# Optimization experiments

Hardware: AMD Instinct MI355X
Metric: run time of the kernel (lower is better)

The kernel has to match this reference:

```python
import jax, jax.numpy as jnp
import numpy as np

B, N, D_IN, D, K, H, ITERS = 128, 4096, 64, 64, 8, 128, 3
SCALE = D ** -0.5
EPS_ATTN = 1e-8
EPS_LN = 1e-5


def layer_norm(x, g, b):
    m = jnp.mean(x, axis=-1, keepdims=True)
    v = jnp.mean((x - m) ** 2, axis=-1, keepdims=True)
    return (x - m) * jax.lax.rsqrt(v + EPS_LN) * g + b


def setup_inputs() -> dict:
    key = jax.random.key(0)
    ks = jax.random.split(key, 16)
    s = 0.05
    return {
        "inputs": jax.random.normal(ks[0], (B, N, D_IN), dtype=jnp.float32),
        "noise": jax.random.normal(ks[1], (B, K, D), dtype=jnp.float32),
        "slots_mu": jax.random.normal(ks[2], (1, 1, D), dtype=jnp.float32),
        "slots_sigma": jax.random.normal(ks[3], (1, 1, D), dtype=jnp.float32),
        "Wq": jax.random.normal(ks[4], (D, D), dtype=jnp.float32) * s,
        "Wk": jax.random.normal(ks[5], (D_IN, D), dtype=jnp.float32) * s,
        "Wv": jax.random.normal(ks[6], (D_IN, D), dtype=jnp.float32) * s,
        "W_ih": jax.random.normal(ks[7], (3 * D, D), dtype=jnp.float32) * s,
        "W_hh": jax.random.normal(ks[8], (3 * D, D), dtype=jnp.float32) * s,
        "b_ih": jnp.zeros((3 * D,), dtype=jnp.float32),
        "b_hh": jnp.zeros((3 * D,), dtype=jnp.float32),
        "mlp_W1": jax.random.normal(ks[9], (D, H), dtype=jnp.float32) * s,
        "mlp_b1": jnp.zeros((H,), dtype=jnp.float32),
        "mlp_W2": jax.random.normal(ks[10], (H, D), dtype=jnp.float32) * s,
        "mlp_b2": jnp.zeros((D,), dtype=jnp.float32),
        "ln_in_g": jnp.ones((D_IN,), dtype=jnp.float32),
        "ln_in_b": jnp.zeros((D_IN,), dtype=jnp.float32),
        "ln_s_g": jnp.ones((D,), dtype=jnp.float32),
        "ln_s_b": jnp.zeros((D,), dtype=jnp.float32),
        "ln_ff_g": jnp.ones((D,), dtype=jnp.float32),
        "ln_ff_b": jnp.zeros((D,), dtype=jnp.float32),
    }


def reference(inputs, noise, slots_mu, slots_sigma, Wq, Wk, Wv,
              W_ih, W_hh, b_ih, b_hh, mlp_W1, mlp_b1, mlp_W2, mlp_b2,
              ln_in_g, ln_in_b, ln_s_g, ln_s_b, ln_ff_g, ln_ff_b):
    # slots = Normal(mu, sigma) with externally supplied standard noise
    slots = slots_mu + slots_sigma * noise                      # [B,K,D]
    x = layer_norm(inputs, ln_in_g, ln_in_b)                     # [B,N,D_IN]
    k = x @ Wk                                                   # [B,N,D]
    v = x @ Wv                                                   # [B,N,D]

    for _ in range(ITERS):
        slots_prev = slots
        s = layer_norm(slots, ln_s_g, ln_s_b)
        q = s @ Wq                                               # [B,K,D]
        dots = jnp.einsum('bid,bjd->bij', q, k) * SCALE          # [B,K,N]
        attn = jax.nn.softmax(dots, axis=1) + EPS_ATTN           # softmax over slots
        attn_n = attn / jnp.sum(attn, axis=-1, keepdims=True)
        updates = jnp.einsum('bjd,bij->bid', v, attn_n)          # [B,K,D]

        # single-step GRU (torch nn.GRU gate order: reset, update, new)
        gx = updates @ W_ih.T + b_ih                             # [B,K,3D]
        gh = slots_prev @ W_hh.T + b_hh                          # [B,K,3D]
        gx_r, gx_z, gx_n = jnp.split(gx, 3, axis=-1)
        gh_r, gh_z, gh_n = jnp.split(gh, 3, axis=-1)
        r = jax.nn.sigmoid(gx_r + gh_r)
        z = jax.nn.sigmoid(gx_z + gh_z)
        n = jnp.tanh(gx_n + r * gh_n)
        slots = (1.0 - z) * n + z * slots_prev

        slots = layer_norm(slots, ln_ff_g, ln_ff_b)
        slots = slots + (jax.nn.relu(slots @ mlp_W1 + mlp_b1) @ mlp_W2 + mlp_b2)
    return slots
```

## Files before the change

### kernel.cpp

```cpp
#include <hip/hip_runtime.h>
#include <hip/hip_bf16.h>

typedef unsigned int u32;
typedef unsigned short u16;
typedef __attribute__((ext_vector_type(8))) short short8;
typedef __attribute__((ext_vector_type(4))) float f32x4;
typedef __attribute__((ext_vector_type(2))) u32 u32x2;

#define B_      128
#define N_      4096
#define K_      8
#define SCALE_  0.125f
#define EPS_A   1e-8f
#define EPS_LN  1e-5f

__device__ __forceinline__ float bf_lo(u32 u){ union{u32 v; float f;} x; x.v = u<<16; return x.f; }
__device__ __forceinline__ u16 f2bf(float f){
  union{float f; u32 v;} x; x.f = f;
  u32 v = x.v;
  return (u16)((v + 0x7fffu + ((v>>16)&1u))>>16);
}
__device__ __forceinline__ float wsum64(float v){
  #pragma unroll
  for (int off=32; off; off>>=1) v += __shfl_xor(v, off, 64);
  return v;
}
__device__ __forceinline__ void gll16(const void* g, void* l){
  __builtin_amdgcn_global_load_lds(
      (const __attribute__((address_space(1))) void*)g,
      (__attribute__((address_space(3))) void*)l, 16, 0, 0);
}

__global__ void prep_t(const float* __restrict__ Wih, const float* __restrict__ Whh,
                       const float* __restrict__ Wq,  const float* __restrict__ Wk,
                       float* __restrict__ WihT, float* __restrict__ WhhT,
                       float* __restrict__ Wqk){
  int t = threadIdx.x;
  if (blockIdx.x < 48){
    int idx = blockIdx.x*256 + t;
    int g = idx>>6, d = idx&63;
    WihT[d*192+g] = Wih[idx];
    WhhT[d*192+g] = Whh[idx];
  } else {
    __shared__ float WkL[64*65];
    int bi = blockIdx.x - 48;
    #pragma unroll
    for (int k=0;k<16;++k){
      int idx = t + k*256;
      int d = idx>>6, m = idx&63;
      WkL[m*65+d] = Wk[idx];
    }
    __syncthreads();
    int a = bi*4 + (t>>6), d = t&63;
    float acc = 0.f;
    #pragma unroll 8
    for (int m=0;m<64;++m) acc += Wq[a*64+m]*WkL[m*65+d];
    Wqk[a*64+d] = acc;
  }
}

__device__ __forceinline__ void tile_attn(
    char* ibuf, char* abuf, short8 qf0, short8 qf1,
    int fr, int fq, f32x4* c2, float* tsl)
{
  f32x4 c1[2];
  #pragma unroll
  for (int nt=0;nt<2;++nt){
    c1[nt] = (f32x4){0.f,0.f,0.f,0.f};
    #pragma unroll
    for (int kk=0;kk<2;++kk){
      int byte = ((kk*2+(fq>>1))<<10) | (((fr>>2)&1)<<9)
               | ((nt*2+(fr>>3))<<7) | ((fr&3)<<5) | ((fq&1)<<4);
      short8 xf = *(const short8*)(ibuf + byte);
      c1[nt] = __builtin_amdgcn_mfma_f32_16x16x32_bf16(kk?qf1:qf0, xf, c1[nt], 0,0,0);
    }
  }
  #pragma unroll
  for (int nt=0;nt<2;++nt){
    float d0 = c1[nt][0]*SCALE_, d1 = c1[nt][1]*SCALE_;
    float d2 = c1[nt][2]*SCALE_, d3 = c1[nt][3]*SCALE_;
    float m = fmaxf(fmaxf(d0,d1), fmaxf(d2,d3));
    m = fmaxf(m, __shfl_xor(m, 16, 64));
    float e0 = __expf(d0-m), e1 = __expf(d1-m), e2 = __expf(d2-m), e3 = __expf(d3-m);
    float sl = e0+e1+e2+e3;
    float inv = 1.f/(sl + __shfl_xor(sl, 16, 64));
    float a0 = e0*inv + EPS_A, a1 = e1*inv + EPS_A;
    float a2 = e2*inv + EPS_A, a3 = e3*inv + EPS_A;
    tsl[0]+=a0; tsl[1]+=a1; tsl[2]+=a2; tsl[3]+=a3;
    int pos2 = (nt*16 + fr)*2;
    *(u16*)(abuf + (((fq*4+0)*64 + pos2) ^ (0<<4))) = f2bf(a0);
    *(u16*)(abuf + (((fq*4+1)*64 + pos2) ^ (1<<4))) = f2bf(a1);
    *(u16*)(abuf + (((fq*4+2)*64 + pos2) ^ (2<<4))) = f2bf(a2);
    *(u16*)(abuf + (((fq*4+3)*64 + pos2) ^ (3<<4))) = f2bf(a3);
  }
  asm volatile("s_waitcnt lgkmcnt(0)" ::: "memory");
  __builtin_amdgcn_sched_barrier(0);
  {
    short8 pa = *(const short8*)(abuf + ((fr*64 + fq*16) ^ ((fr&3)<<4)));
    u32 va = (u32)(size_t)ibuf + (fq<<7) + (fr<<1);
    u32x2 tv0,tv1,tv2,tv3,tv4,tv5,tv6,tv7;
    asm volatile("ds_read_b64_tr_b16 %0, %1 offset:0"    : "=v"(tv0) : "v"(va));
    asm volatile("ds_read_b64_tr_b16 %0, %1 offset:512"  : "=v"(tv1) : "v"(va));
    asm volatile("ds_read_b64_tr_b16 %0, %1 offset:1024" : "=v"(tv2) : "v"(va));
    asm volatile("ds_read_b64_tr_b16 %0, %1 offset:1536" : "=v"(tv3) : "v"(va));
    asm volatile("ds_read_b64_tr_b16 %0, %1 offset:2048" : "=v"(tv4) : "v"(va));
    asm volatile("ds_read_b64_tr_b16 %0, %1 offset:2560" : "=v"(tv5) : "v"(va));
    asm volatile("ds_read_b64_tr_b16 %0, %1 offset:3072" : "=v"(tv6) : "v"(va));
    asm volatile("ds_read_b64_tr_b16 %0, %1 offset:3584" : "=v"(tv7) : "v"(va));
    asm volatile("s_waitcnt lgkmcnt(0)" ::: "memory");
    __builtin_amdgcn_sched_barrier(0);
    union { short8 s8; u32 u4[4]; } xb;
    xb.u4[0]=tv0.x; xb.u4[1]=tv0.y; xb.u4[2]=tv1.x; xb.u4[3]=tv1.y;
    c2[0] = __builtin_amdgcn_mfma_f32_16x16x32_bf16(pa, xb.s8, c2[0], 0,0,0);
    xb.u4[0]=tv2.x; xb.u4[1]=tv2.y; xb.u4[2]=tv3.x; xb.u4[3]=tv3.y;
    c2[1] = __builtin_amdgcn_mfma_f32_16x16x32_bf16(pa, xb.s8, c2[1], 0,0,0);
    xb.u4[0]=tv4.x; xb.u4[1]=tv4.y; xb.u4[2]=tv5.x; xb.u4[3]=tv5.y;
    c2[2] = __builtin_amdgcn_mfma_f32_16x16x32_bf16(pa, xb.s8, c2[2], 0,0,0);
    xb.u4[0]=tv6.x; xb.u4[1]=tv6.y; xb.u4[2]=tv7.x; xb.u4[3]=tv7.y;
    c2[3] = __builtin_amdgcn_mfma_f32_16x16x32_bf16(pa, xb.s8, c2[3], 0,0,0);
  }
}

__global__ __launch_bounds__(512,1) void fused_sa(
    const float* __restrict__ inp, u16* __restrict__ xhat,
    const float* __restrict__ noise, const float* __restrict__ mu, const float* __restrict__ sigma,
    const float* __restrict__ Wqk,
    const float* __restrict__ lng, const float* __restrict__ lnb,
    const float* __restrict__ lnsg, const float* __restrict__ lnsb,
    const float* __restrict__ WihT, const float* __restrict__ WhhT,
    const float* __restrict__ bih, const float* __restrict__ bhh,
    const float* __restrict__ W1, const float* __restrict__ b1,
    const float* __restrict__ W2, const float* __restrict__ b2,
    const float* __restrict__ lnffg, const float* __restrict__ lnffb,
    const float* __restrict__ Wv,
    float* __restrict__ dout)
{
  __shared__ __align__(16) char smem[152320];
  int b = blockIdx.x, t = threadIdx.x;
  int w = t>>6, lane = t&63;
  int fr = lane&15, fq = lane>>4;
  int i = w, d = lane;

  char*  wbase = smem + w*9216;
  char*  abuf  = wbase + 8192;
  char*  qA    = smem + 73728;
  float* UL    = (float*)(smem + 75776);
  float* SL    = (float*)(smem + 92160);
  u16*   wih_l = (u16*)(smem + 92416);
  u16*   whh_l = (u16*)(smem + 116992);
  float* updL  = (float*)(smem + 141568);
  float* spL   = (float*)(smem + 143744);
  float* sfL   = (float*)(smem + 145920);
  float* hL    = (float*)(smem + 148096);

  {
    const float4* wa = (const float4*)WihT;
    const float4* wb = (const float4*)WhhT;
    #pragma unroll
    for (int k2=0;k2<6;++k2){
      int idx = t + k2*512;
      float4 va = wa[idx], vb = wb[idx];
      ((u32*)wih_l)[idx*2]   = (u32)f2bf(va.x) | ((u32)f2bf(va.y)<<16);
      ((u32*)wih_l)[idx*2+1] = (u32)f2bf(va.z) | ((u32)f2bf(va.w)<<16);
      ((u32*)whh_l)[idx*2]   = (u32)f2bf(vb.x) | ((u32)f2bf(vb.y)<<16);
      ((u32*)whh_l)[idx*2+1] = (u32)f2bf(vb.z) | ((u32)f2bf(vb.w)<<16);
    }
  }
  if (t < 256) ((u32*)(qA + 1024))[t] = 0;
  float sp = mu[d] + sigma[d]*noise[b*512 + t];
  {
    float m  = wsum64(sp)*(1.f/64.f);
    float df = sp - m;
    float vv = wsum64(df*df)*(1.f/64.f);
    float sv = df*rsqrtf(vv+EPS_LN)*lnsg[d] + lnsb[d];
    updL[i*68+d] = sv;
  }
  __syncthreads();
  {
    float qt = 0.f;
    #pragma unroll 8
    for (int dd=0; dd<64; ++dd) qt += updL[i*68+dd]*Wqk[dd*64 + d];
    *(u16*)(qA + ((i*128 + d*2) ^ ((i&7)<<4))) = f2bf(qt);
  }
  __syncthreads();

  long tbase = (long)b*128 + w*16;

  for (int it=0; it<3; ++it){
    f32x4 c2[4];
    #pragma unroll
    for (int k2=0;k2<4;++k2) c2[k2] = (f32x4){0.f,0.f,0.f,0.f};
    float tsl[4] = {0.f,0.f,0.f,0.f};
    short8 qf0 = *(const short8*)(qA + ((fr*128 +  0 + fq*16) ^ ((fr&7)<<4)));
    short8 qf1 = *(const short8*)(qA + ((fr*128 + 64 + fq*16) ^ ((fr&7)<<4)));

    if (it == 0){
      for (int tile=0; tile<16; ++tile){
        char* ibuf = wbase;
        {
          int r = lane>>1, h = lane&1;
          const float4* xr = (const float4*)(inp + ((long)b*N_ + w*512 + tile*32 + r)*64 + h*32);
          float xv[32]; float s=0.f, sq=0.f;
          #pragma unroll
          for (int c=0;c<8;++c){
            float4 f = xr[c];
            xv[c*4+0]=f.x; xv[c*4+1]=f.y; xv[c*4+2]=f.z; xv[c*4+3]=f.w;
            s  += f.x+f.y+f.z+f.w;
            sq += f.x*f.x+f.y*f.y+f.z*f.z+f.w*f.w;
          }
          s  += __shfl_xor(s,1,64);
          sq += __shfl_xor(sq,1,64);
          float mean = s*(1.f/64.f);
          float inv  = rsqrtf(sq*(1.f/64.f) - mean*mean + EPS_LN);
          float lgv[32], lbv[32];
          {
            const float4* g4 = (const float4*)(lng + h*32);
            const float4* b4 = (const float4*)(lnb + h*32);
            #pragma unroll
            for (int e=0;e<8;++e){
              float4 gv = g4[e], bv = b4[e];
              lgv[e*4+0]=gv.x; lgv[e*4+1]=gv.y; lgv[e*4+2]=gv.z; lgv[e*4+3]=gv.w;
              lbv[e*4+0]=bv.x; lbv[e*4+1]=bv.y; lbv[e*4+2]=bv.z; lbv[e*4+3]=bv.w;
            }
          }
          u32 pk[16];
          #pragma unroll
          for (int e=0;e<16;++e){
            float a0 = (xv[e*2]  -mean)*inv*lgv[e*2]   + lbv[e*2];
            float a1 = (xv[e*2+1]-mean)*inv*lgv[e*2+1] + lbv[e*2+1];
            pk[e] = (u32)f2bf(a0) | ((u32)f2bf(a1)<<16);
          }
          int pbits = (((r>>2)&1)<<9) | (((r>>3)&3)<<7) | ((r&3)<<5);
          #pragma unroll
          for (int half=0; half<2; ++half){
            int dt = h*2 + half;
            uint4 v0; v0.x=pk[half*8+0]; v0.y=pk[half*8+1]; v0.z=pk[half*8+2]; v0.w=pk[half*8+3];
            uint4 v1; v1.x=pk[half*8+4]; v1.y=pk[half*8+5]; v1.z=pk[half*8+6]; v1.w=pk[half*8+7];
            *(uint4*)(ibuf + ((dt<<10) | pbits))      = v0;
            *(uint4*)(ibuf + ((dt<<10) | pbits) + 16) = v1;
          }
          asm volatile("s_waitcnt lgkmcnt(0)" ::: "memory");
          __builtin_amdgcn_sched_barrier(0);
          char* gim = (char*)xhat + ((tbase+tile)<<12) + lane*16;
          #pragma unroll
          for (int j=0;j<4;++j)
            *(uint4*)(gim + j*1024) = *(const uint4*)(ibuf + lane*16 + j*1024);
        }
        tile_attn(ibuf, abuf, qf0, qf1, fr, fq, c2, tsl);
      }
      asm volatile("s_waitcnt vmcnt(0)" ::: "memory");
      __builtin_amdgcn_sched_barrier(0);
    } else {
      {
        const char* g0 = (const char*)xhat + (tbase<<12) + lane*16;
        #pragma unroll
        for (int j=0;j<4;++j) gll16(g0 + j*1024, wbase + j*1024);
      }
      #pragma unroll 2
      for (int tile=0; tile<16; ++tile){
        char* ibuf = wbase + (tile&1)*4096;
        if (tile < 15){
          const char* gn = (const char*)xhat + ((tbase+tile+1)<<12) + lane*16;
          char* ln = wbase + ((tile+1)&1)*4096;
          #pragma unroll
          for (int j=0;j<4;++j) gll16(gn + j*1024, ln + j*1024);
          asm volatile("s_waitcnt vmcnt(4)" ::: "memory");
        } else {
          asm volatile("s_waitcnt vmcnt(0)" ::: "memory");
        }
        __builtin_amdgcn_sched_barrier(0);
        tile_attn(ibuf, abuf, qf0, qf1, fr, fq, c2, tsl);
      }
    }
    if (fq < 2){
      #pragma unroll
      for (int dblk=0;dblk<4;++dblk){
        #pragma unroll
        for (int r=0;r<4;++r)
          UL[w*512 + (fq*4+r)*64 + dblk*16 + fr] = c2[dblk][r];
      }
    }
    #pragma unroll
    for (int mk=1; mk<16; mk<<=1){
      tsl[0] += __shfl_xor(tsl[0], mk, 64);
      tsl[1] += __shfl_xor(tsl[1], mk, 64);
      tsl[2] += __shfl_xor(tsl[2], mk, 64);
      tsl[3] += __shfl_xor(tsl[3], mk, 64);
    }
    if (fr==0 && fq<2){
      SL[w*8 + fq*4+0] = tsl[0]; SL[w*8 + fq*4+1] = tsl[1];
      SL[w*8 + fq*4+2] = tsl[2]; SL[w*8 + fq*4+3] = tsl[3];
    }
    __syncthreads();

    float u = 0.f, S = 0.f;
    #pragma unroll
    for (int cw=0; cw<8; ++cw){
      u += UL[cw*512 + i*64 + d];
      S += SL[cw*8 + i];
    }
    float ut = u / S;
    sfL[i*68+d] = ut;
    spL[i*68+d] = sp;
    __syncthreads();
    float upd = 0.f;
    #pragma unroll 8
    for (int dd=0; dd<64; ++dd) upd += sfL[i*68+dd]*Wv[dd*64 + d];
    updL[i*68+d] = upd;
    __syncthreads();
    float gx0 = bih[d], gx1 = bih[64+d], gx2 = bih[128+d];
    float gh0 = bhh[d], gh1 = bhh[64+d], gh2 = bhh[128+d];
    #pragma unroll 8
    for (int dd=0; dd<64; ++dd){
      float uv = updL[i*68+dd];
      float sv = spL[i*68+dd];
      gx0 += uv*bf_lo((u32)wih_l[dd*192 + d]);
      gx1 += uv*bf_lo((u32)wih_l[dd*192 + 64 + d]);
      gx2 += uv*bf_lo((u32)wih_l[dd*192 + 128 + d]);
      gh0 += sv*bf_lo((u32)whh_l[dd*192 + d]);
      gh1 += sv*bf_lo((u32)whh_l[dd*192 + 64 + d]);
      gh2 += sv*bf_lo((u32)whh_l[dd*192 + 128 + d]);
    }
    float rg = 1.f/(1.f+__expf(-(gx0+gh0)));
    float zg = 1.f/(1.f+__expf(-(gx1+gh1)));
    float ng = tanhf(gx2 + rg*gh2);
    float sn = (1.f-zg)*ng + zg*sp;
    float m1 = wsum64(sn)*(1.f/64.f);
    float df = sn-m1;
    float vv = wsum64(df*df)*(1.f/64.f);
    float sf = df*rsqrtf(vv+EPS_LN)*lnffg[d] + lnffb[d];
    sfL[i*68+d] = sf;
    __syncthreads();
    float h0 = b1[d], h1 = b1[64+d];
    #pragma unroll 8
    for (int dd=0;dd<64;++dd){
      float sv = sfL[i*68+dd];
      h0 += sv*W1[dd*128 + d];
      h1 += sv*W1[dd*128 + 64 + d];
    }
    h0 = fmaxf(h0, 0.f); h1 = fmaxf(h1, 0.f);
    hL[i*132+d] = h0; hL[i*132+64+d] = h1;
    __syncthreads();
    float o = b2[d];
    #pragma unroll 8
    for (int hh=0; hh<128; ++hh) o += hL[i*132+hh]*W2[hh*64 + d];
    float out = sf + o;
    sp = out;
    if (it == 2){
      dout[b*512 + t] = out;
    } else {
      float m2 = wsum64(out)*(1.f/64.f);
      float d2 = out-m2;
      float v2 = wsum64(d2*d2)*(1.f/64.f);
      float sq = d2*rsqrtf(v2+EPS_LN)*lnsg[d] + lnsb[d];
      updL[i*68+d] = sq;
      __syncthreads();
      float qt = 0.f;
      #pragma unroll 8
      for (int dd=0;dd<64;++dd) qt += updL[i*68+dd]*Wqk[dd*64 + d];
      *(u16*)(qA + ((i*128 + d*2) ^ ((i&7)<<4))) = f2bf(qt);
      __syncthreads();
    }
  }
}

extern "C" void kernel_launch(void* const* d_in, const int* in_sizes, int n_in,
                              void* d_out, int out_size, void* d_ws, size_t ws_size,
                              hipStream_t stream){
  const float* inp   = (const float*)d_in[0];
  const float* noise = (const float*)d_in[1];
  const float* mu    = (const float*)d_in[2];
  const float* sigma = (const float*)d_in[3];
  const float* Wq    = (const float*)d_in[4];
  const float* Wk    = (const float*)d_in[5];
  const float* Wv    = (const float*)d_in[6];
  const float* Wih   = (const float*)d_in[7];
  const float* Whh   = (const float*)d_in[8];
  const float* bih   = (const float*)d_in[9];
  const float* bhh   = (const float*)d_in[10];
  const float* W1    = (const float*)d_in[11];
  const float* b1    = (const float*)d_in[12];
  const float* W2    = (const float*)d_in[13];
  const float* b2    = (const float*)d_in[14];
  const float* lnig  = (const float*)d_in[15];
  const float* lnib  = (const float*)d_in[16];
  const float* lnsg  = (const float*)d_in[17];
  const float* lnsb  = (const float*)d_in[18];
  const float* lnffg = (const float*)d_in[19];
  const float* lnffb = (const float*)d_in[20];
  float* out = (float*)d_out;

  char* ws = (char*)d_ws;
  u16*   xhat = (u16*)(ws);
  float* WihT = (float*)(ws + 67108864);
  float* WhhT = (float*)(ws + 67158016);
  float* Wqk  = (float*)(ws + 67207168);

  prep_t<<<64,256,0,stream>>>(Wih, Whh, Wq, Wk, WihT, WhhT, Wqk);
  fused_sa<<<B_,512,0,stream>>>(inp, xhat, noise, mu, sigma, Wqk,
                                lnig, lnib, lnsg, lnsb,
                                WihT, WhhT, bih, bhh,
                                W1, b1, W2, b2, lnffg, lnffb, Wv, out);
}
```

Baseline: 137.1 us.

## Split each batch across two workgroups with a global flag handshake for partial sums

Each batch's N dimension is now split between two workgroups, giving 256 blocks instead of 128 so more of the CUs are busy. The two halves exchange their partial update and softmax-denominator sums through global memory, synchronising on a per-batch atomic counter that is spin-waited once per iteration. Both halves then redundantly compute the small GRU/MLP slot update. The spin-wait assumes both blocks of a pair are resident at the same time, which holds only if all 256 blocks fit on the device at once; otherwise it can deadlock.

```diff
diff --git a/kernel.cpp b/kernel.cpp
--- a/kernel.cpp
+++ b/kernel.cpp
@@ -34,8 +34,9 @@
 __global__ void prep_t(const float* __restrict__ Wih, const float* __restrict__ Whh,
                        const float* __restrict__ Wq,  const float* __restrict__ Wk,
                        float* __restrict__ WihT, float* __restrict__ WhhT,
-                       float* __restrict__ Wqk){
+                       float* __restrict__ Wqk, int* __restrict__ flags){
   int t = threadIdx.x;
+  if (blockIdx.x == 0 && t < B_) flags[t] = 0;
   if (blockIdx.x < 48){
     int idx = blockIdx.x*256 + t;
     int g = idx>>6, d = idx&63;
@@ -133,10 +134,12 @@
     const float* __restrict__ W2, const float* __restrict__ b2,
     const float* __restrict__ lnffg, const float* __restrict__ lnffb,
     const float* __restrict__ Wv,
+    float* __restrict__ PUg, float* __restrict__ PSg, int* __restrict__ flags,
     float* __restrict__ dout)
 {
   __shared__ __align__(16) char smem[152320];
-  int b = blockIdx.x, t = threadIdx.x;
+  int bid = blockIdx.x, t = threadIdx.x;
+  int b = bid>>1, half = bid&1;
   int w = t>>6, lane = t&63;
   int fr = lane&15, fq = lane>>4;
   int i = w, d = lane;
@@ -184,7 +187,7 @@
   }
   __syncthreads();
 
-  long tbase = (long)b*128 + w*16;
+  long tbase = (long)b*128 + half*64 + w*8;
 
   for (int it=0; it<3; ++it){
     f32x4 c2[4];
@@ -195,11 +198,12 @@
     short8 qf1 = *(const short8*)(qA + ((fr*128 + 64 + fq*16) ^ ((fr&7)<<4)));
 
     if (it == 0){
-      for (int tile=0; tile<16; ++tile){
+      for (int tile=0; tile<8; ++tile){
         char* ibuf = wbase;
         {
-          int r = lane>>1, h = lane&1;
-          const float4* xr = (const float4*)(inp + ((long)b*N_ + w*512 + tile*32 + r)*64 + h*32);
+          int r = lane>>1, hx = lane&1;
+          const float4* xr = (const float4*)(inp +
+              ((long)b*N_ + half*2048 + w*256 + tile*32 + r)*64 + hx*32);
           float xv[32]; float s=0.f, sq=0.f;
           #pragma unroll
           for (int c=0;c<8;++c){
@@ -214,8 +218,8 @@
           float inv  = rsqrtf(sq*(1.f/64.f) - mean*mean + EPS_LN);
           float lgv[32], lbv[32];
           {
-            const float4* g4 = (const float4*)(lng + h*32);
-            const float4* b4 = (const float4*)(lnb + h*32);
+            const float4* g4 = (const float4*)(lng + hx*32);
+            const float4* b4 = (const float4*)(lnb + hx*32);
             #pragma unroll
             for (int e=0;e<8;++e){
               float4 gv = g4[e], bv = b4[e];
@@ -232,10 +236,10 @@
           }
           int pbits = (((r>>2)&1)<<9) | (((r>>3)&3)<<7) | ((r&3)<<5);
           #pragma unroll
-          for (int half=0; half<2; ++half){
-            int dt = h*2 + half;
-            uint4 v0; v0.x=pk[half*8+0]; v0.y=pk[half*8+1]; v0.z=pk[half*8+2]; v0.w=pk[half*8+3];
-            uint4 v1; v1.x=pk[half*8+4]; v1.y=pk[half*8+5]; v1.z=pk[half*8+6]; v1.w=pk[half*8+7];
+          for (int hf=0; hf<2; ++hf){
+            int dt = hx*2 + hf;
+            uint4 v0; v0.x=pk[hf*8+0]; v0.y=pk[hf*8+1]; v0.z=pk[hf*8+2]; v0.w=pk[hf*8+3];
+            uint4 v1; v1.x=pk[hf*8+4]; v1.y=pk[hf*8+5]; v1.z=pk[hf*8+6]; v1.w=pk[hf*8+7];
             *(uint4*)(ibuf + ((dt<<10) | pbits))      = v0;
             *(uint4*)(ibuf + ((dt<<10) | pbits) + 16) = v1;
           }
@@ -257,9 +261,9 @@
         for (int j=0;j<4;++j) gll16(g0 + j*1024, wbase + j*1024);
       }
       #pragma unroll 2
-      for (int tile=0; tile<16; ++tile){
+      for (int tile=0; tile<8; ++tile){
         char* ibuf = wbase + (tile&1)*4096;
-        if (tile < 15){
+        if (tile < 7){
           const char* gn = (const char*)xhat + ((tbase+tile+1)<<12) + lane*16;
           char* ln = wbase + ((tile+1)&1)*4096;
           #pragma unroll
@@ -299,6 +303,24 @@
       u += UL[cw*512 + i*64 + d];
       S += SL[cw*8 + i];
     }
+    {
+      long pbase = ((long)(it&1)*B_*2 + b*2 + half);
+      __hip_atomic_store(&PUg[pbase*512 + t], u, __ATOMIC_RELEASE, __HIP_MEMORY_SCOPE_AGENT);
+      if (d == 0)
+        __hip_atomic_store(&PSg[pbase*8 + i], S, __ATOMIC_RELEASE, __HIP_MEMORY_SCOPE_AGENT);
+    }
+    __syncthreads();
+    if (t == 0){
+      __hip_atomic_fetch_add(&flags[b], 1, __ATOMIC_ACQ_REL, __HIP_MEMORY_SCOPE_AGENT);
+      while (__hip_atomic_load(&flags[b], __ATOMIC_ACQUIRE, __HIP_MEMORY_SCOPE_AGENT) < 2*(it+1)) { }
+    }
+    __syncthreads();
+    {
+      long obase = ((long)(it&1)*B_*2 + b*2 + (half^1));
+      u += __hip_atomic_load(&PUg[obase*512 + t], __ATOMIC_ACQUIRE, __HIP_MEMORY_SCOPE_AGENT);
+      S += __hip_atomic_load(&PSg[obase*8 + i], __ATOMIC_ACQUIRE, __HIP_MEMORY_SCOPE_AGENT);
+    }
+
     float ut = u / S;
     sfL[i*68+d] = ut;
     spL[i*68+d] = sp;
@@ -347,7 +369,7 @@
     float out = sf + o;
     sp = out;
     if (it == 2){
-      dout[b*512 + t] = out;
+      if (half == 0) dout[b*512 + t] = out;
     } else {
       float m2 = wsum64(out)*(1.f/64.f);
       float d2 = out-m2;
@@ -391,14 +413,18 @@
   float* out = (float*)d_out;
 
   char* ws = (char*)d_ws;
-  u16*   xhat = (u16*)(ws);
-  float* WihT = (float*)(ws + 67108864);
-  float* WhhT = (float*)(ws + 67158016);
-  float* Wqk  = (float*)(ws + 67207168);
-
-  prep_t<<<64,256,0,stream>>>(Wih, Whh, Wq, Wk, WihT, WhhT, Wqk);
-  fused_sa<<<B_,512,0,stream>>>(inp, xhat, noise, mu, sigma, Wqk,
-                                lnig, lnib, lnsg, lnsb,
-                                WihT, WhhT, bih, bhh,
-                                W1, b1, W2, b2, lnffg, lnffb, Wv, out);
-}
+  u16*   xhat  = (u16*)(ws);
+  float* WihT  = (float*)(ws + 67108864);
+  float* WhhT  = (float*)(ws + 67158016);
+  float* Wqk   = (float*)(ws + 67207168);
+  float* PUg   = (float*)(ws + 67223552);
+  float* PSg   = (float*)(ws + 68272128);
+  int*   flags = (int*)(ws + 68288512);
+
+  prep_t<<<64,256,0,stream>>>(Wih, Whh, Wq, Wk, WihT, WhhT, Wqk, flags);
+  fused_sa<<<2*B_,512,0,stream>>>(inp, xhat, noise, mu, sigma, Wqk,
+                                  lnig, lnib, lnsg, lnsb,
+                                  WihT, WhhT, bih, bhh,
+                                  W1, b1, W2, b2, lnffg, lnffb, Wv,
+                                  PUg, PSg, flags, out);
+}
```

Result: slower. 320.0 us (+133.5%).

## Double block to 1024 threads splitting N across 16 waves, drop LDS GRU weights

Applied to the files above, without the earlier changes.

Launches 1024 threads per batch element so 16 waves each handle 256 tokens instead of 8 waves handling 512, doubling the parallelism of the attention sweep. To fit in LDS, the bf16 copies of the GRU weights are removed and read directly from global fp32. Per-wave partial U/S results are reused inside each wave's buffer, and the slot-update phase runs on only the first 512 threads. This adds register pressure and more barriers, and the GRU matvec now reads global memory.

```diff
diff --git a/kernel.cpp b/kernel.cpp
--- a/kernel.cpp
+++ b/kernel.cpp
@@ -121,7 +121,7 @@
   }
 }
 
-__global__ __launch_bounds__(512,1) void fused_sa(
+__global__ __launch_bounds__(1024,1) void fused_sa(
     const float* __restrict__ inp, u16* __restrict__ xhat,
     const float* __restrict__ noise, const float* __restrict__ mu, const float* __restrict__ sigma,
     const float* __restrict__ Wqk,
@@ -135,40 +135,24 @@
     const float* __restrict__ Wv,
     float* __restrict__ dout)
 {
-  __shared__ __align__(16) char smem[152320];
+  __shared__ __align__(16) char smem[149504];
   int b = blockIdx.x, t = threadIdx.x;
   int w = t>>6, lane = t&63;
   int fr = lane&15, fq = lane>>4;
-  int i = w, d = lane;
+  int i = (t>>6)&7, d = lane;
 
   char*  wbase = smem + w*9216;
   char*  abuf  = wbase + 8192;
-  char*  qA    = smem + 73728;
-  float* UL    = (float*)(smem + 75776);
-  float* SL    = (float*)(smem + 92160);
-  u16*   wih_l = (u16*)(smem + 92416);
-  u16*   whh_l = (u16*)(smem + 116992);
-  float* updL  = (float*)(smem + 141568);
-  float* spL   = (float*)(smem + 143744);
-  float* sfL   = (float*)(smem + 145920);
-  float* hL    = (float*)(smem + 148096);
-
-  {
-    const float4* wa = (const float4*)WihT;
-    const float4* wb = (const float4*)WhhT;
-    #pragma unroll
-    for (int k2=0;k2<6;++k2){
-      int idx = t + k2*512;
-      float4 va = wa[idx], vb = wb[idx];
-      ((u32*)wih_l)[idx*2]   = (u32)f2bf(va.x) | ((u32)f2bf(va.y)<<16);
-      ((u32*)wih_l)[idx*2+1] = (u32)f2bf(va.z) | ((u32)f2bf(va.w)<<16);
-      ((u32*)whh_l)[idx*2]   = (u32)f2bf(vb.x) | ((u32)f2bf(vb.y)<<16);
-      ((u32*)whh_l)[idx*2+1] = (u32)f2bf(vb.z) | ((u32)f2bf(vb.w)<<16);
-    }
-  }
+  char*  qA    = smem + 147456;
+  float* updL  = (float*)(smem +  8*9216 + 4096);
+  float* spL   = (float*)(smem +  9*9216 + 4096);
+  float* sfL   = (float*)(smem + 10*9216 + 4096);
+  float* hL    = (float*)(smem + 11*9216 + 4096);
+
   if (t < 256) ((u32*)(qA + 1024))[t] = 0;
-  float sp = mu[d] + sigma[d]*noise[b*512 + t];
-  {
+  float sp = 0.f;
+  if (t < 512){
+    sp = mu[d] + sigma[d]*noise[b*512 + t];
     float m  = wsum64(sp)*(1.f/64.f);
     float df = sp - m;
     float vv = wsum64(df*df)*(1.f/64.f);
@@ -176,7 +160,7 @@
     updL[i*68+d] = sv;
   }
   __syncthreads();
-  {
+  if (t < 512){
     float qt = 0.f;
     #pragma unroll 8
     for (int dd=0; dd<64; ++dd) qt += updL[i*68+dd]*Wqk[dd*64 + d];
@@ -184,7 +168,7 @@
   }
   __syncthreads();
 
-  long tbase = (long)b*128 + w*16;
+  long tbase = (long)b*128 + w*8;
 
   for (int it=0; it<3; ++it){
     f32x4 c2[4];
@@ -195,11 +179,12 @@
     short8 qf1 = *(const short8*)(qA + ((fr*128 + 64 + fq*16) ^ ((fr&7)<<4)));
 
     if (it == 0){
-      for (int tile=0; tile<16; ++tile){
+      for (int tile=0; tile<8; ++tile){
         char* ibuf = wbase;
         {
-          int r = lane>>1, h = lane&1;
-          const float4* xr = (const float4*)(inp + ((long)b*N_ + w*512 + tile*32 + r)*64 + h*32);
+          int r = lane>>1, hx = lane&1;
+          const float4* xr = (const float4*)(inp +
+              ((long)b*N_ + w*256 + tile*32 + r)*64 + hx*32);
           float xv[32]; float s=0.f, sq=0.f;
           #pragma unroll
           for (int c=0;c<8;++c){
@@ -214,8 +199,8 @@
           float inv  = rsqrtf(sq*(1.f/64.f) - mean*mean + EPS_LN);
           float lgv[32], lbv[32];
           {
-            const float4* g4 = (const float4*)(lng + h*32);
-            const float4* b4 = (const float4*)(lnb + h*32);
+            const float4* g4 = (const float4*)(lng + hx*32);
+            const float4* b4 = (const float4*)(lnb + hx*32);
             #pragma unroll
             for (int e=0;e<8;++e){
               float4 gv = g4[e], bv = b4[e];
@@ -232,10 +217,10 @@
           }
           int pbits = (((r>>2)&1)<<9) | (((r>>3)&3)<<7) | ((r&3)<<5);
           #pragma unroll
-          for (int half=0; half<2; ++half){
-            int dt = h*2 + half;
-            uint4 v0; v0.x=pk[half*8+0]; v0.y=pk[half*8+1]; v0.z=pk[half*8+2]; v0.w=pk[half*8+3];
-            uint4 v1; v1.x=pk[half*8+4]; v1.y=pk[half*8+5]; v1.z=pk[half*8+6]; v1.w=pk[half*8+7];
+          for (int hf=0; hf<2; ++hf){
+            int dt = hx*2 + hf;
+            uint4 v0; v0.x=pk[hf*8+0]; v0.y=pk[hf*8+1]; v0.z=pk[hf*8+2]; v0.w=pk[hf*8+3];
+            uint4 v1; v1.x=pk[hf*8+4]; v1.y=pk[hf*8+5]; v1.z=pk[hf*8+6]; v1.w=pk[hf*8+7];
             *(uint4*)(ibuf + ((dt<<10) | pbits))      = v0;
             *(uint4*)(ibuf + ((dt<<10) | pbits) + 16) = v1;
           }
@@ -257,9 +242,9 @@
         for (int j=0;j<4;++j) gll16(g0 + j*1024, wbase + j*1024);
       }
       #pragma unroll 2
-      for (int tile=0; tile<16; ++tile){
+      for (int tile=0; tile<8; ++tile){
         char* ibuf = wbase + (tile&1)*4096;
-        if (tile < 15){
+        if (tile < 7){
           const char* gn = (const char*)xhat + ((tbase+tile+1)<<12) + lane*16;
           char* ln = wbase + ((tile+1)&1)*4096;
           #pragma unroll
@@ -272,93 +257,113 @@
         tile_attn(ibuf, abuf, qf0, qf1, fr, fq, c2, tsl);
       }
     }
-    if (fq < 2){
+    {
+      float* ULw = (float*)wbase;
+      float* SLw = (float*)(wbase + 2048);
+      if (fq < 2){
+        #pragma unroll
+        for (int dblk=0;dblk<4;++dblk){
+          #pragma unroll
+          for (int r=0;r<4;++r)
+            ULw[(fq*4+r)*64 + dblk*16 + fr] = c2[dblk][r];
+        }
+      }
       #pragma unroll
-      for (int dblk=0;dblk<4;++dblk){
-        #pragma unroll
-        for (int r=0;r<4;++r)
-          UL[w*512 + (fq*4+r)*64 + dblk*16 + fr] = c2[dblk][r];
-      }
-    }
-    #pragma unroll
-    for (int mk=1; mk<16; mk<<=1){
-      tsl[0] += __shfl_xor(tsl[0], mk, 64);
-      tsl[1] += __shfl_xor(tsl[1], mk, 64);
-      tsl[2] += __shfl_xor(tsl[2], mk, 64);
-      tsl[3] += __shfl_xor(tsl[3], mk, 64);
-    }
-    if (fr==0 && fq<2){
-      SL[w*8 + fq*4+0] = tsl[0]; SL[w*8 + fq*4+1] = tsl[1];
-      SL[w*8 + fq*4+2] = tsl[2]; SL[w*8 + fq*4+3] = tsl[3];
-    }
-    __syncthreads();
-
-    float u = 0.f, S = 0.f;
-    #pragma unroll
-    for (int cw=0; cw<8; ++cw){
-      u += UL[cw*512 + i*64 + d];
-      S += SL[cw*8 + i];
-    }
-    float ut = u / S;
-    sfL[i*68+d] = ut;
-    spL[i*68+d] = sp;
-    __syncthreads();
-    float upd = 0.f;
-    #pragma unroll 8
-    for (int dd=0; dd<64; ++dd) upd += sfL[i*68+dd]*Wv[dd*64 + d];
-    updL[i*68+d] = upd;
-    __syncthreads();
-    float gx0 = bih[d], gx1 = bih[64+d], gx2 = bih[128+d];
-    float gh0 = bhh[d], gh1 = bhh[64+d], gh2 = bhh[128+d];
-    #pragma unroll 8
-    for (int dd=0; dd<64; ++dd){
-      float uv = updL[i*68+dd];
-      float sv = spL[i*68+dd];
-      gx0 += uv*bf_lo((u32)wih_l[dd*192 + d]);
-      gx1 += uv*bf_lo((u32)wih_l[dd*192 + 64 + d]);
-      gx2 += uv*bf_lo((u32)wih_l[dd*192 + 128 + d]);
-      gh0 += sv*bf_lo((u32)whh_l[dd*192 + d]);
-      gh1 += sv*bf_lo((u32)whh_l[dd*192 + 64 + d]);
-      gh2 += sv*bf_lo((u32)whh_l[dd*192 + 128 + d]);
-    }
-    float rg = 1.f/(1.f+__expf(-(gx0+gh0)));
-    float zg = 1.f/(1.f+__expf(-(gx1+gh1)));
-    float ng = tanhf(gx2 + rg*gh2);
-    float sn = (1.f-zg)*ng + zg*sp;
-    float m1 = wsum64(sn)*(1.f/64.f);
-    float df = sn-m1;
-    float vv = wsum64(df*df)*(1.f/64.f);
-    float sf = df*rsqrtf(vv+EPS_LN)*lnffg[d] + lnffb[d];
-    sfL[i*68+d] = sf;
-    __syncthreads();
-    float h0 = b1[d], h1 = b1[64+d];
-    #pragma unroll 8
-    for (int dd=0;dd<64;++dd){
-      float sv = sfL[i*68+dd];
-      h0 += sv*W1[dd*128 + d];
-      h1 += sv*W1[dd*128 + 64 + d];
-    }
-    h0 = fmaxf(h0, 0.f); h1 = fmaxf(h1, 0.f);
-    hL[i*132+d] = h0; hL[i*132+64+d] = h1;
-    __syncthreads();
-    float o = b2[d];
-    #pragma unroll 8
-    for (int hh=0; hh<128; ++hh) o += hL[i*132+hh]*W2[hh*64 + d];
-    float out = sf + o;
-    sp = out;
-    if (it == 2){
-      dout[b*512 + t] = out;
-    } else {
-      float m2 = wsum64(out)*(1.f/64.f);
-      float d2 = out-m2;
-      float v2 = wsum64(d2*d2)*(1.f/64.f);
-      float sq = d2*rsqrtf(v2+EPS_LN)*lnsg[d] + lnsb[d];
-      updL[i*68+d] = sq;
-      __syncthreads();
-      float qt = 0.f;
+      for (int mk=1; mk<16; mk<<=1){
+        tsl[0] += __shfl_xor(tsl[0], mk, 64);
+        tsl[1] += __shfl_xor(tsl[1], mk, 64);
+        tsl[2] += __shfl_xor(tsl[2], mk, 64);
+        tsl[3] += __shfl_xor(tsl[3], mk, 64);
+      }
+      if (fr==0 && fq<2){
+        SLw[fq*4+0] = tsl[0]; SLw[fq*4+1] = tsl[1];
+        SLw[fq*4+2] = tsl[2]; SLw[fq*4+3] = tsl[3];
+      }
+    }
+    __syncthreads();
+
+    if (t < 512){
+      float u = 0.f, S = 0.f;
+      #pragma unroll
+      for (int cw=0; cw<16; ++cw){
+        u += ((const float*)(smem + cw*9216))[i*64 + d];
+        S += ((const float*)(smem + cw*9216 + 2048))[i];
+      }
+      float ut = u / S;
+      sfL[i*68+d] = ut;
+      spL[i*68+d] = sp;
+    }
+    __syncthreads();
+    if (t < 512){
+      float upd = 0.f;
       #pragma unroll 8
-      for (int dd=0;dd<64;++dd) qt += updL[i*68+dd]*Wqk[dd*64 + d];
-      *(u16*)(qA + ((i*128 + d*2) ^ ((i&7)<<4))) = f2bf(qt);
+      for (int dd=0; dd<64; ++dd) upd += sfL[i*68+dd]*Wv[dd*64 + d];
+      updL[i*68+d] = upd;
+    }
+    __syncthreads();
+    float out = 0.f;
+    if (t < 512){
+      float gx0 = bih[d], gx1 = bih[64+d], gx2 = bih[128+d];
+      float gh0 = bhh[d], gh1 = bhh[64+d], gh2 = bhh[128+d];
+      #pragma unroll 8
+      for (int dd=0; dd<64; ++dd){
+        float uv = updL[i*68+dd];
+        float sv = spL[i*68+dd];
+        gx0 += uv*WihT[dd*192 + d];
+        gx1 += uv*WihT[dd*192 + 64 + d];
+        gx2 += uv*WihT[dd*192 + 128 + d];
+        gh0 += sv*WhhT[dd*192 + d];
+        gh1 += sv*WhhT[dd*192 + 64 + d];
+        gh2 += sv*WhhT[dd*192 + 128 + d];
+      }
+      float rg = 1.f/(1.f+__expf(-(gx0+gh0)));
+      float zg = 1.f/(1.f+__expf(-(gx1+gh1)));
+      float ng = tanhf(gx2 + rg*gh2);
+      float sn = (1.f-zg)*ng + zg*sp;
+      float m1 = wsum64(sn)*(1.f/64.f);
+      float df = sn-m1;
+      float vv = wsum64(df*df)*(1.f/64.f);
+      float sf = df*rsqrtf(vv+EPS_LN)*lnffg[d] + lnffb[d];
+      sfL[i*68+d] = sf;
+      out = sf;
+    }
+    __syncthreads();
+    if (t < 512){
+      float h0 = b1[d], h1 = b1[64+d];
+      #pragma unroll 8
+      for (int dd=0;dd<64;++dd){
+        float sv = sfL[i*68+dd];
+        h0 += sv*W1[dd*128 + d];
+        h1 += sv*W1[dd*128 + 64 + d];
+      }
+      h0 = fmaxf(h0, 0.f); h1 = fmaxf(h1, 0.f);
+      hL[i*132+d] = h0; hL[i*132+64+d] = h1;
+    }
+    __syncthreads();
+    if (t < 512){
+      float o = b2[d];
+      #pragma unroll 8
+      for (int hh=0; hh<128; ++hh) o += hL[i*132+hh]*W2[hh*64 + d];
+      out = out + o;
+      sp = out;
+      if (it == 2){
+        dout[b*512 + t] = out;
+      } else {
+        float m2 = wsum64(out)*(1.f/64.f);
+        float d2 = out-m2;
+        float v2 = wsum64(d2*d2)*(1.f/64.f);
+        float sq = d2*rsqrtf(v2+EPS_LN)*lnsg[d] + lnsb[d];
+        updL[i*68+d] = sq;
+      }
+    }
+    __syncthreads();
+    if (it < 2){
+      if (t < 512){
+        float qt = 0.f;
+        #pragma unroll 8
+        for (int dd=0;dd<64;++dd) qt += updL[i*68+dd]*Wqk[dd*64 + d];
+        *(u16*)(qA + ((i*128 + d*2) ^ ((i&7)<<4))) = f2bf(qt);
+      }
       __syncthreads();
     }
   }
@@ -397,8 +402,8 @@
   float* Wqk  = (float*)(ws + 67207168);
 
   prep_t<<<64,256,0,stream>>>(Wih, Whh, Wq, Wk, WihT, WhhT, Wqk);
-  fused_sa<<<B_,512,0,stream>>>(inp, xhat, noise, mu, sigma, Wqk,
-                                lnig, lnib, lnsg, lnsb,
-                                WihT, WhhT, bih, bhh,
-                                W1, b1, W2, b2, lnffg, lnffb, Wv, out);
-}
+  fused_sa<<<B_,1024,0,stream>>>(inp, xhat, noise, mu, sigma, Wqk,
+                                 lnig, lnib, lnsg, lnsb,
+                                 WihT, WhhT, bih, bhh,
+                                 W1, b1, W2, b2, lnffg, lnffb, Wv, out);
+}
```

Measured after the change: 312.4 us. +127.9%, slower.
